# Kernel tuning notes

Measured on AMD Instinct MI355X. Metric: run time of the kernel, lower is better.

Reference implementation:

```python
import jax, jax.numpy as jnp
import numpy as np

D_MODEL = 1024
HEADS = 16
D_K = D_MODEL // HEADS
B, S = 4, 2048


def setup_inputs() -> dict:
    key = jax.random.key(0)
    ks = jax.random.split(key, 12)
    xav = float(np.sqrt(6.0 / (D_MODEL + D_MODEL)))  # xavier_uniform bound
    inp = {
        "query": jax.random.normal(ks[0], (B, S, D_MODEL), jnp.float32),
        "key": jax.random.normal(ks[1], (B, S, D_MODEL), jnp.float32),
        "value": jax.random.normal(ks[2], (B, S, D_MODEL), jnp.float32),
        # causal mask, broadcast over batch and heads: [1,1,S,S]
        "mask": jnp.tril(jnp.ones((S, S), jnp.int32))[None, None],
        "Wq": jax.random.uniform(ks[3], (D_MODEL, D_MODEL), jnp.float32, -xav, xav),
        "bq": jnp.zeros((D_MODEL,), jnp.float32),
        "Wk": jax.random.uniform(ks[4], (D_MODEL, D_MODEL), jnp.float32, -xav, xav),
        "bk": jnp.zeros((D_MODEL,), jnp.float32),
        "Wv": jax.random.uniform(ks[5], (D_MODEL, D_MODEL), jnp.float32, -xav, xav),
        "bv": jnp.zeros((D_MODEL,), jnp.float32),
        "Wo": jax.random.uniform(ks[6], (D_MODEL, D_MODEL), jnp.float32, -xav, xav),
        "bo": jnp.zeros((D_MODEL,), jnp.float32),
    }
    return inp


def reference(query, key, value, mask, Wq, bq, Wk, bk, Wv, bv, Wo, bo):
    b, s, d = query.shape
    # torch Linear: y = x @ W.T + b, W is [out, in]
    Q = (jnp.einsum("bsd,ed->bse", query, Wq) + bq).reshape(b, s, HEADS, D_K).transpose(0, 2, 1, 3)
    K = (jnp.einsum("bsd,ed->bse", key, Wk) + bk).reshape(b, -1, HEADS, D_K).transpose(0, 2, 1, 3)
    V = (jnp.einsum("bsd,ed->bse", value, Wv) + bv).reshape(b, -1, HEADS, D_K).transpose(0, 2, 1, 3)
    scale = 1.0 / jnp.sqrt(jnp.asarray(D_K, query.dtype))
    scores = jnp.einsum("bhqd,bhkd->bhqk", Q, K) * scale  # [B,H,S,S]
    scores = jnp.where(mask == 0, -jnp.inf, scores)
    attn = jax.nn.softmax(scores, axis=-1)
    attn = jnp.where(jnp.isnan(attn), jnp.zeros_like(attn), attn)  # nan-fix as in source
    out = jnp.einsum("bhqk,bhkd->bhqd", attn, V)
    out = out.transpose(0, 2, 1, 3).reshape(b, s, d)
    return jnp.einsum("bsd,ed->bse", out, Wo) + bo
```

## Files before the change

kernel.cpp:

```cpp
#include <hip/hip_runtime.h>
#include <hip/hip_bf16.h>

#define DM 1024
#define NHEADS 16
#define DKH 64
#define BATCH 4
#define SEQ 2048
#define MROWS (BATCH*SEQ)

typedef __attribute__((ext_vector_type(8))) short bf16x8;
typedef __attribute__((ext_vector_type(4))) short bf16x4;
typedef __attribute__((ext_vector_type(4))) float f32x4;

#if __has_builtin(__builtin_amdgcn_exp2f)
#define EXP2(x) __builtin_amdgcn_exp2f(x)
#else
#define EXP2(x) exp2f(x)
#endif

__device__ __forceinline__ unsigned short f2bf(float f){
  unsigned u = __float_as_uint(f);
  u += 0x7fffu + ((u >> 16) & 1u);
  return (unsigned short)(u >> 16);
}

__device__ __forceinline__ void gload16(const unsigned short* g, unsigned short* l){
  __builtin_amdgcn_global_load_lds((const __attribute__((address_space(1))) void*)g,
                                   (__attribute__((address_space(3))) void*)l, 16, 0, 0);
}

struct ConvArgs { const float* src[7]; unsigned short* dst[7]; };

__global__ __launch_bounds__(256) void conv_all(ConvArgs a){
  const int bx = blockIdx.x;
  int t, boff;
  if (bx < 24576){ t = bx >> 13; boff = bx & 8191; }
  else { int j = bx - 24576; t = 3 + (j >> 10); boff = j & 1023; }
  const float* __restrict__ src = a.src[t];
  unsigned short* __restrict__ dst = a.dst[t];
  const int i = (boff * 256 + threadIdx.x) * 4;
  const float4 v = *reinterpret_cast<const float4*>(src + i);
  ushort4 o;
  o.x = f2bf(v.x); o.y = f2bf(v.y); o.z = f2bf(v.z); o.w = f2bf(v.w);
  *reinterpret_cast<ushort4*>(dst + i) = o;
}

template<int MODE>
__global__ __launch_bounds__(256)
void gemm_bt(const unsigned short* __restrict__ A, const unsigned short* __restrict__ Bw,
             const float* __restrict__ bias, void* __restrict__ out, float scale)
{
  const int K = 1024;
  __shared__ short a_sh[128*64];
  __shared__ short b_sh[128*64];
  const int tid  = threadIdx.x;
  const int lane = tid & 63;
  const int wid  = tid >> 6;
  const int wm = wid >> 1, wn = wid & 1;
  const int tileM = blockIdx.x * 128;
  const int tileN = blockIdx.y * 128;

  f32x4 acc[4][4];
  #pragma unroll
  for (int i = 0; i < 4; i++)
    #pragma unroll
    for (int j = 0; j < 4; j++)
      acc[i][j] = (f32x4){0.f,0.f,0.f,0.f};

  const int lr = lane & 15;
  const int lg = lane >> 4;

  for (int k0 = 0; k0 < K; k0 += 64){
    bf16x8 ra[4], rb[4];
    #pragma unroll
    for (int i = 0; i < 4; i++){
      int v   = tid + 256*i;
      int row = v >> 3;
      int cg  = v & 7;
      ra[i] = *reinterpret_cast<const bf16x8*>(A  + (size_t)(tileM+row)*K + k0 + cg*8);
      rb[i] = *reinterpret_cast<const bf16x8*>(Bw + (size_t)(tileN+row)*K + k0 + cg*8);
    }
    __syncthreads();
    #pragma unroll
    for (int i = 0; i < 4; i++){
      int v   = tid + 256*i;
      int row = v >> 3;
      int cg  = v & 7;
      *reinterpret_cast<bf16x8*>(&a_sh[row*64 + ((cg ^ (row & 7)) * 8)]) = ra[i];
      *reinterpret_cast<bf16x8*>(&b_sh[row*64 + ((cg ^ (row & 7)) * 8)]) = rb[i];
    }
    __syncthreads();
    #pragma unroll
    for (int kk = 0; kk < 64; kk += 32){
      bf16x8 af[4], bfr[4];
      const int g0 = lg + (kk >> 3);
      #pragma unroll
      for (int fm = 0; fm < 4; fm++){
        int row = wm*64 + fm*16 + lr;
        af[fm] = *reinterpret_cast<const bf16x8*>(&a_sh[row*64 + ((g0 ^ (row & 7)) * 8)]);
      }
      #pragma unroll
      for (int fn = 0; fn < 4; fn++){
        int row = wn*64 + fn*16 + lr;
        bfr[fn] = *reinterpret_cast<const bf16x8*>(&b_sh[row*64 + ((g0 ^ (row & 7)) * 8)]);
      }
      #pragma unroll
      for (int fm = 0; fm < 4; fm++)
        #pragma unroll
        for (int fn = 0; fn < 4; fn++)
          acc[fm][fn] = __builtin_amdgcn_mfma_f32_16x16x32_bf16(af[fm], bfr[fn], acc[fm][fn], 0, 0, 0);
    }
  }

  #pragma unroll
  for (int fm = 0; fm < 4; fm++){
    #pragma unroll
    for (int fn = 0; fn < 4; fn++){
      #pragma unroll
      for (int r = 0; r < 4; r++){
        int m = tileM + wm*64 + fm*16 + lg*4 + r;
        int n = tileN + wn*64 + fn*16 + lr;
        float val = acc[fm][fn][r] + bias[n];
        if (MODE == 0){
          val *= scale;
          int b = m >> 11, s = m & 2047, h = n >> 6, d = n & 63;
          ((unsigned short*)out)[(((size_t)(b*NHEADS + h)*SEQ + s)*DKH + d)] = f2bf(val);
        } else if (MODE == 1){
          int b = m >> 11, s = m & 2047, h = n >> 6, d = n & 63;
          ((unsigned short*)out)[(((size_t)(b*NHEADS + h)*DKH + d)*SEQ + s)] = f2bf(val);
        } else {
          ((float*)out)[(size_t)m*DM + n] = val;
        }
      }
    }
  }
}

__global__ __launch_bounds__(256)
void attn_kernel(const unsigned short* __restrict__ Q, const unsigned short* __restrict__ Kb,
                 const unsigned short* __restrict__ Vt, unsigned short* __restrict__ Oout)
{
  __shared__ unsigned short k_sh[2][64*64];
  __shared__ unsigned short v_sh[2][64*64];
  const int lane = threadIdx.x & 63;
  const int w    = threadIdx.x >> 6;
  const int lr = lane & 15, grp = lane >> 4;
  const int bh = blockIdx.x;
  const int qtile = 15 - (int)blockIdx.y;
  const int qb0 = qtile * 128;
  const int qw0 = qb0 + w * 32;
  const int b = bh >> 4, h = bh & 15;
  const size_t kbase = (size_t)bh * SEQ * DKH;
  const size_t vbase = (size_t)bh * DKH * SEQ;

  const int r8 = lane >> 3, c8 = lane & 7;
  const int rowS0 = w*16 + r8;
  const int rowS1 = w*16 + 8 + r8;
  const size_t offK0 = (size_t)rowS0*DKH  + (size_t)((c8 ^ (rowS0 & 7)) * 8);
  const size_t offK1 = (size_t)rowS1*DKH  + (size_t)((c8 ^ (rowS1 & 7)) * 8);
  const size_t offV0 = (size_t)rowS0*SEQ  + (size_t)((c8 ^ (rowS0 & 7)) * 8);
  const size_t offV1 = (size_t)rowS1*SEQ  + (size_t)((c8 ^ (rowS1 & 7)) * 8);
  const int ldsA = (w*16)*64;
  const int ldsB = (w*16+8)*64;

  bf16x8 qf[2][2];
  #pragma unroll
  for (int qg = 0; qg < 2; qg++){
    size_t off = kbase + (size_t)(qw0 + qg*16 + lr)*DKH + grp*8;
    qf[qg][0] = *reinterpret_cast<const bf16x8*>(Q + off);
    qf[qg][1] = *reinterpret_cast<const bf16x8*>(Q + off + 32);
  }

  bf16x4 ones4;
  ones4[0] = (short)0x3F80; ones4[1] = (short)0x3F80;
  ones4[2] = (short)0x3F80; ones4[3] = (short)0x3F80;

  float mrun[2] = {-__builtin_inff(), -__builtin_inff()};
  f32x4 ls[2];
  f32x4 o[2][4];
  #pragma unroll
  for (int qg = 0; qg < 2; qg++){
    ls[qg] = (f32x4){0.f,0.f,0.f,0.f};
    #pragma unroll
    for (int dc = 0; dc < 4; dc++) o[qg][dc] = (f32x4){0.f,0.f,0.f,0.f};
  }

  const int nkb = qb0/64 + 2;

#define STAGE(kb_, bf_) do { \
    gload16(Kb + kbase + (size_t)(kb_)*4096 + offK0, (unsigned short*)&k_sh[bf_][ldsA]); \
    gload16(Kb + kbase + (size_t)(kb_)*4096 + offK1, (unsigned short*)&k_sh[bf_][ldsB]); \
    gload16(Vt + vbase + (size_t)(kb_)*64   + offV0, (unsigned short*)&v_sh[bf_][ldsA]); \
    gload16(Vt + vbase + (size_t)(kb_)*64   + offV1, (unsigned short*)&v_sh[bf_][ldsB]); \
  } while(0)

  STAGE(0, 0);
  __syncthreads();

  for (int kb = 0; kb < nkb; kb++){
    const int buf = kb & 1;
    if (kb + 1 < nkb) STAGE(kb + 1, buf ^ 1);

    if (kb*64 <= qw0 + 31){
      const unsigned short* ks = k_sh[buf];
      const unsigned short* vs = v_sh[buf];
      const bool act0 = (kb*64 <= qw0 + 15);

      f32x4 st[2][4];
      __builtin_amdgcn_s_setprio(1);
      #pragma unroll
      for (int ksub = 0; ksub < 4; ksub++){
        int rowk = ksub*16 + lr;
        bf16x8 kf0 = *reinterpret_cast<const bf16x8*>(&ks[rowk*64 + ((grp ^ (rowk & 7)) * 8)]);
        bf16x8 kf1 = *reinterpret_cast<const bf16x8*>(&ks[rowk*64 + (((4 + grp) ^ (rowk & 7)) * 8)]);
        #pragma unroll
        for (int qg = 0; qg < 2; qg++){
          f32x4 s = (f32x4){0.f,0.f,0.f,0.f};
          s = __builtin_amdgcn_mfma_f32_16x16x32_bf16(kf0, qf[qg][0], s, 0, 0, 0);
          s = __builtin_amdgcn_mfma_f32_16x16x32_bf16(kf1, qf[qg][1], s, 0, 0, 0);
          st[qg][ksub] = s;
        }
      }
      __builtin_amdgcn_s_setprio(0);

      bf16x4 pb[2][4];
      #pragma unroll
      for (int qg = 0; qg < 2; qg++){
        if (qg == 0 && !act0) continue;
        const int qgb = qw0 + qg*16;
        if (kb*64 + 63 > qgb){
          #pragma unroll
          for (int ksub = 0; ksub < 4; ksub++)
            #pragma unroll
            for (int r = 0; r < 4; r++){
              int kg = kb*64 + ksub*16 + grp*4 + r;
              if (kg > qgb + lr) st[qg][ksub][r] = -__builtin_inff();
            }
        }
        float mt = fmaxf(fmaxf(st[qg][0][0], st[qg][0][1]), fmaxf(st[qg][0][2], st[qg][0][3]));
        #pragma unroll
        for (int ksub = 1; ksub < 4; ksub++){
          mt = fmaxf(mt, fmaxf(fmaxf(st[qg][ksub][0], st[qg][ksub][1]),
                               fmaxf(st[qg][ksub][2], st[qg][ksub][3])));
        }
        mt = fmaxf(mt, __shfl_xor(mt, 16));
        mt = fmaxf(mt, __shfl_xor(mt, 32));
        const float mnew = fmaxf(mrun[qg], mt);
        const float corr = EXP2(mrun[qg] - mnew);
        mrun[qg] = mnew;
        #pragma unroll
        for (int dc = 0; dc < 4; dc++){
          o[qg][dc][0] *= corr; o[qg][dc][1] *= corr;
          o[qg][dc][2] *= corr; o[qg][dc][3] *= corr;
        }
        ls[qg][0] *= corr;
        #pragma unroll
        for (int ksub = 0; ksub < 4; ksub++){
          float p0 = EXP2(st[qg][ksub][0] - mnew);
          float p1 = EXP2(st[qg][ksub][1] - mnew);
          float p2 = EXP2(st[qg][ksub][2] - mnew);
          float p3 = EXP2(st[qg][ksub][3] - mnew);
          pb[qg][ksub][0] = (short)f2bf(p0);
          pb[qg][ksub][1] = (short)f2bf(p1);
          pb[qg][ksub][2] = (short)f2bf(p2);
          pb[qg][ksub][3] = (short)f2bf(p3);
        }
      }

      __builtin_amdgcn_s_setprio(1);
      #pragma unroll
      for (int ksub = 0; ksub < 4; ksub++){
        #pragma unroll
        for (int dc = 0; dc < 4; dc++){
          int rowd = dc*16 + lr;
          int cg16 = ksub*2 + (grp >> 1);
          bf16x4 vf = *reinterpret_cast<const bf16x4*>(
              &vs[rowd*64 + ((cg16 ^ (rowd & 7)) * 8) + (grp & 1)*4]);
          if (act0) o[0][dc] = __builtin_amdgcn_mfma_f32_16x16x16bf16_1k(vf, pb[0][ksub], o[0][dc], 0, 0, 0);
          o[1][dc] = __builtin_amdgcn_mfma_f32_16x16x16bf16_1k(vf, pb[1][ksub], o[1][dc], 0, 0, 0);
        }
        if (act0) ls[0] = __builtin_amdgcn_mfma_f32_16x16x16bf16_1k(ones4, pb[0][ksub], ls[0], 0, 0, 0);
        ls[1] = __builtin_amdgcn_mfma_f32_16x16x16bf16_1k(ones4, pb[1][ksub], ls[1], 0, 0, 0);
      }
      __builtin_amdgcn_s_setprio(0);
    }
    __syncthreads();
  }
#undef STAGE

  #pragma unroll
  for (int qg = 0; qg < 2; qg++){
    float inv = 1.0f / ls[qg][0];
    int qglob = qw0 + qg*16 + lr;
    size_t ob = ((size_t)(b*SEQ + qglob))*DM + h*DKH;
    #pragma unroll
    for (int dc = 0; dc < 4; dc++){
      ushort4 pk;
      pk.x = f2bf(o[qg][dc][0]*inv);
      pk.y = f2bf(o[qg][dc][1]*inv);
      pk.z = f2bf(o[qg][dc][2]*inv);
      pk.w = f2bf(o[qg][dc][3]*inv);
      *reinterpret_cast<ushort4*>(&Oout[ob + dc*16 + grp*4]) = pk;
    }
  }
}

extern "C" void kernel_launch(void* const* d_in, const int* in_sizes, int n_in,
                              void* d_out, int out_size, void* d_ws, size_t ws_size,
                              hipStream_t stream) {
  const float* query = (const float*)d_in[0];
  const float* key   = (const float*)d_in[1];
  const float* value = (const float*)d_in[2];
  const float* Wq = (const float*)d_in[4];
  const float* bq = (const float*)d_in[5];
  const float* Wk = (const float*)d_in[6];
  const float* bk = (const float*)d_in[7];
  const float* Wv = (const float*)d_in[8];
  const float* bv = (const float*)d_in[9];
  const float* Wo = (const float*)d_in[10];
  const float* bo = (const float*)d_in[11];
  float* out = (float*)d_out;

  char* ws = (char*)d_ws;
  const size_t SZ_X = (size_t)MROWS * DM * 2;
  const size_t SZ_W = (size_t)DM * DM * 2;
  unsigned short* qb  = (unsigned short*)(ws + 0);
  unsigned short* kb  = (unsigned short*)(ws + SZ_X);
  unsigned short* vb  = (unsigned short*)(ws + 2*SZ_X);
  unsigned short* wqb = (unsigned short*)(ws + 3*SZ_X);
  unsigned short* wkb = (unsigned short*)(ws + 3*SZ_X + SZ_W);
  unsigned short* wvb = (unsigned short*)(ws + 3*SZ_X + 2*SZ_W);
  unsigned short* wob = (unsigned short*)(ws + 3*SZ_X + 3*SZ_W);
  unsigned short* Vt  = (unsigned short*)(ws + 3*SZ_X + 4*SZ_W);
  unsigned short* Qb   = vb;
  unsigned short* Kbuf = qb;
  unsigned short* attO = kb;

  ConvArgs ca;
  ca.src[0] = query; ca.src[1] = key; ca.src[2] = value;
  ca.src[3] = Wq; ca.src[4] = Wk; ca.src[5] = Wv; ca.src[6] = Wo;
  ca.dst[0] = qb; ca.dst[1] = kb; ca.dst[2] = vb;
  ca.dst[3] = wqb; ca.dst[4] = wkb; ca.dst[5] = wvb; ca.dst[6] = wob;
  conv_all<<<28672, 256, 0, stream>>>(ca);

  dim3 gg(MROWS/128, DM/128);
  const float qscale = 0.125f * 1.4426950408889634f;
  gemm_bt<1><<<gg, 256, 0, stream>>>(vb, wvb, bv, (void*)Vt,   1.0f);
  gemm_bt<0><<<gg, 256, 0, stream>>>(qb, wqb, bq, (void*)Qb,   qscale);
  gemm_bt<0><<<gg, 256, 0, stream>>>(kb, wkb, bk, (void*)Kbuf, 1.0f);

  attn_kernel<<<dim3(64, 16), 256, 0, stream>>>(Qb, Kbuf, Vt, attO);

  gemm_bt<2><<<gg, 256, 0, stream>>>(attO, wob, bo, (void*)out, 1.0f);
}
```

Before: 216.6 us.

## Fuse fp32-to-bf16 activation conversion into projection GEMM loads; restructure attention softmax loop

Stops converting the query/key/value activations to bf16 in a separate pass. The QKV projection GEMMs now read the fp32 activations directly and convert them in registers with packed bf16 conversions, which removes a large write-then-read round trip through memory. Only the weights go through the standalone conversion kernel, and the workspace layout is rearranged to match. The attention kernel also gets a launch-bounds occupancy hint, computes the scores one query group at a time to cut register pressure, and uses packed bf16 conversion for the probabilities. In exchange the GEMMs fetch twice as many activation bytes per tile.

```diff
diff --git a/kernel.cpp b/kernel.cpp
--- a/kernel.cpp
+++ b/kernel.cpp
@@ -24,18 +24,31 @@
   return (unsigned short)(u >> 16);
 }
 
+__device__ __forceinline__ unsigned pk2bf(float lo, float hi){
+  union { __hip_bfloat162 h; unsigned u; } c;
+  c.h = __float22bfloat162_rn(make_float2(lo, hi));
+  return c.u;
+}
+
+__device__ __forceinline__ bf16x8 cvtA8(float4 a, float4 b){
+  union { unsigned u[4]; bf16x8 v; } r;
+  r.u[0] = pk2bf(a.x, a.y);
+  r.u[1] = pk2bf(a.z, a.w);
+  r.u[2] = pk2bf(b.x, b.y);
+  r.u[3] = pk2bf(b.z, b.w);
+  return r.v;
+}
+
 __device__ __forceinline__ void gload16(const unsigned short* g, unsigned short* l){
   __builtin_amdgcn_global_load_lds((const __attribute__((address_space(1))) void*)g,
                                    (__attribute__((address_space(3))) void*)l, 16, 0, 0);
 }
 
-struct ConvArgs { const float* src[7]; unsigned short* dst[7]; };
-
-__global__ __launch_bounds__(256) void conv_all(ConvArgs a){
-  const int bx = blockIdx.x;
-  int t, boff;
-  if (bx < 24576){ t = bx >> 13; boff = bx & 8191; }
-  else { int j = bx - 24576; t = 3 + (j >> 10); boff = j & 1023; }
+struct ConvArgs { const float* src[4]; unsigned short* dst[4]; };
+
+__global__ __launch_bounds__(256) void conv_w(ConvArgs a){
+  const int t = blockIdx.x >> 10;
+  const int boff = blockIdx.x & 1023;
   const float* __restrict__ src = a.src[t];
   unsigned short* __restrict__ dst = a.dst[t];
   const int i = (boff * 256 + threadIdx.x) * 4;
@@ -45,9 +58,9 @@
   *reinterpret_cast<ushort4*>(dst + i) = o;
 }
 
-template<int MODE>
+template<int MODE, int AFP32>
 __global__ __launch_bounds__(256)
-void gemm_bt(const unsigned short* __restrict__ A, const unsigned short* __restrict__ Bw,
+void gemm_bt(const void* __restrict__ Av, const unsigned short* __restrict__ Bw,
              const float* __restrict__ bias, void* __restrict__ out, float scale)
 {
   const int K = 1024;
@@ -77,7 +90,14 @@
       int v   = tid + 256*i;
       int row = v >> 3;
       int cg  = v & 7;
-      ra[i] = *reinterpret_cast<const bf16x8*>(A  + (size_t)(tileM+row)*K + k0 + cg*8);
+      if constexpr (AFP32){
+        const float* Af = (const float*)Av;
+        const float4 f0 = *reinterpret_cast<const float4*>(Af + (size_t)(tileM+row)*K + k0 + cg*8);
+        const float4 f1 = *reinterpret_cast<const float4*>(Af + (size_t)(tileM+row)*K + k0 + cg*8 + 4);
+        ra[i] = cvtA8(f0, f1);
+      } else {
+        ra[i] = *reinterpret_cast<const bf16x8*>((const unsigned short*)Av + (size_t)(tileM+row)*K + k0 + cg*8);
+      }
       rb[i] = *reinterpret_cast<const bf16x8*>(Bw + (size_t)(tileN+row)*K + k0 + cg*8);
     }
     __syncthreads();
@@ -136,7 +156,7 @@
   }
 }
 
-__global__ __launch_bounds__(256)
+__global__ __launch_bounds__(256, 4)
 void attn_kernel(const unsigned short* __restrict__ Q, const unsigned short* __restrict__ Kb,
                  const unsigned short* __restrict__ Vt, unsigned short* __restrict__ Oout)
 {
@@ -206,27 +226,24 @@
       const unsigned short* vs = v_sh[buf];
       const bool act0 = (kb*64 <= qw0 + 15);
 
-      f32x4 st[2][4];
-      __builtin_amdgcn_s_setprio(1);
-      #pragma unroll
-      for (int ksub = 0; ksub < 4; ksub++){
-        int rowk = ksub*16 + lr;
-        bf16x8 kf0 = *reinterpret_cast<const bf16x8*>(&ks[rowk*64 + ((grp ^ (rowk & 7)) * 8)]);
-        bf16x8 kf1 = *reinterpret_cast<const bf16x8*>(&ks[rowk*64 + (((4 + grp) ^ (rowk & 7)) * 8)]);
-        #pragma unroll
-        for (int qg = 0; qg < 2; qg++){
+      bf16x4 pb[2][4];
+      #pragma unroll
+      for (int qg = 0; qg < 2; qg++){
+        if (qg == 0 && !act0) continue;
+        f32x4 st[4];
+        __builtin_amdgcn_s_setprio(1);
+        #pragma unroll
+        for (int ksub = 0; ksub < 4; ksub++){
+          int rowk = ksub*16 + lr;
+          bf16x8 kf0 = *reinterpret_cast<const bf16x8*>(&ks[rowk*64 + ((grp ^ (rowk & 7)) * 8)]);
+          bf16x8 kf1 = *reinterpret_cast<const bf16x8*>(&ks[rowk*64 + (((4 + grp) ^ (rowk & 7)) * 8)]);
           f32x4 s = (f32x4){0.f,0.f,0.f,0.f};
           s = __builtin_amdgcn_mfma_f32_16x16x32_bf16(kf0, qf[qg][0], s, 0, 0, 0);
           s = __builtin_amdgcn_mfma_f32_16x16x32_bf16(kf1, qf[qg][1], s, 0, 0, 0);
-          st[qg][ksub] = s;
-        }
-      }
-      __builtin_amdgcn_s_setprio(0);
-
-      bf16x4 pb[2][4];
-      #pragma unroll
-      for (int qg = 0; qg < 2; qg++){
-        if (qg == 0 && !act0) continue;
+          st[ksub] = s;
+        }
+        __builtin_amdgcn_s_setprio(0);
+
         const int qgb = qw0 + qg*16;
         if (kb*64 + 63 > qgb){
           #pragma unroll
@@ -234,14 +251,14 @@
             #pragma unroll
             for (int r = 0; r < 4; r++){
               int kg = kb*64 + ksub*16 + grp*4 + r;
-              if (kg > qgb + lr) st[qg][ksub][r] = -__builtin_inff();
+              if (kg > qgb + lr) st[ksub][r] = -__builtin_inff();
             }
         }
-        float mt = fmaxf(fmaxf(st[qg][0][0], st[qg][0][1]), fmaxf(st[qg][0][2], st[qg][0][3]));
+        float mt = fmaxf(fmaxf(st[0][0], st[0][1]), fmaxf(st[0][2], st[0][3]));
         #pragma unroll
         for (int ksub = 1; ksub < 4; ksub++){
-          mt = fmaxf(mt, fmaxf(fmaxf(st[qg][ksub][0], st[qg][ksub][1]),
-                               fmaxf(st[qg][ksub][2], st[qg][ksub][3])));
+          mt = fmaxf(mt, fmaxf(fmaxf(st[ksub][0], st[ksub][1]),
+                               fmaxf(st[ksub][2], st[ksub][3])));
         }
         mt = fmaxf(mt, __shfl_xor(mt, 16));
         mt = fmaxf(mt, __shfl_xor(mt, 32));
@@ -256,14 +273,14 @@
         ls[qg][0] *= corr;
         #pragma unroll
         for (int ksub = 0; ksub < 4; ksub++){
-          float p0 = EXP2(st[qg][ksub][0] - mnew);
-          float p1 = EXP2(st[qg][ksub][1] - mnew);
-          float p2 = EXP2(st[qg][ksub][2] - mnew);
-          float p3 = EXP2(st[qg][ksub][3] - mnew);
-          pb[qg][ksub][0] = (short)f2bf(p0);
-          pb[qg][ksub][1] = (short)f2bf(p1);
-          pb[qg][ksub][2] = (short)f2bf(p2);
-          pb[qg][ksub][3] = (short)f2bf(p3);
+          float p0 = EXP2(st[ksub][0] - mnew);
+          float p1 = EXP2(st[ksub][1] - mnew);
+          float p2 = EXP2(st[ksub][2] - mnew);
+          float p3 = EXP2(st[ksub][3] - mnew);
+          union { unsigned u[2]; bf16x4 v; } pk;
+          pk.u[0] = pk2bf(p0, p1);
+          pk.u[1] = pk2bf(p2, p3);
+          pb[qg][ksub] = pk.v;
         }
       }
 
@@ -324,32 +341,27 @@
   char* ws = (char*)d_ws;
   const size_t SZ_X = (size_t)MROWS * DM * 2;
   const size_t SZ_W = (size_t)DM * DM * 2;
-  unsigned short* qb  = (unsigned short*)(ws + 0);
-  unsigned short* kb  = (unsigned short*)(ws + SZ_X);
-  unsigned short* vb  = (unsigned short*)(ws + 2*SZ_X);
-  unsigned short* wqb = (unsigned short*)(ws + 3*SZ_X);
-  unsigned short* wkb = (unsigned short*)(ws + 3*SZ_X + SZ_W);
-  unsigned short* wvb = (unsigned short*)(ws + 3*SZ_X + 2*SZ_W);
-  unsigned short* wob = (unsigned short*)(ws + 3*SZ_X + 3*SZ_W);
-  unsigned short* Vt  = (unsigned short*)(ws + 3*SZ_X + 4*SZ_W);
-  unsigned short* Qb   = vb;
-  unsigned short* Kbuf = qb;
-  unsigned short* attO = kb;
+  unsigned short* wqb = (unsigned short*)(ws + 0);
+  unsigned short* wkb = (unsigned short*)(ws + SZ_W);
+  unsigned short* wvb = (unsigned short*)(ws + 2*SZ_W);
+  unsigned short* wob = (unsigned short*)(ws + 3*SZ_W);
+  unsigned short* Qb   = (unsigned short*)(ws + 4*SZ_W);
+  unsigned short* Kbuf = (unsigned short*)(ws + 4*SZ_W + SZ_X);
+  unsigned short* Vt   = (unsigned short*)(ws + 4*SZ_W + 2*SZ_X);
+  unsigned short* attO = (unsigned short*)(ws + 4*SZ_W + 3*SZ_X);
 
   ConvArgs ca;
-  ca.src[0] = query; ca.src[1] = key; ca.src[2] = value;
-  ca.src[3] = Wq; ca.src[4] = Wk; ca.src[5] = Wv; ca.src[6] = Wo;
-  ca.dst[0] = qb; ca.dst[1] = kb; ca.dst[2] = vb;
-  ca.dst[3] = wqb; ca.dst[4] = wkb; ca.dst[5] = wvb; ca.dst[6] = wob;
-  conv_all<<<28672, 256, 0, stream>>>(ca);
+  ca.src[0] = Wq; ca.src[1] = Wk; ca.src[2] = Wv; ca.src[3] = Wo;
+  ca.dst[0] = wqb; ca.dst[1] = wkb; ca.dst[2] = wvb; ca.dst[3] = wob;
+  conv_w<<<4096, 256, 0, stream>>>(ca);
 
   dim3 gg(MROWS/128, DM/128);
   const float qscale = 0.125f * 1.4426950408889634f;
-  gemm_bt<1><<<gg, 256, 0, stream>>>(vb, wvb, bv, (void*)Vt,   1.0f);
-  gemm_bt<0><<<gg, 256, 0, stream>>>(qb, wqb, bq, (void*)Qb,   qscale);
-  gemm_bt<0><<<gg, 256, 0, stream>>>(kb, wkb, bk, (void*)Kbuf, 1.0f);
+  gemm_bt<1,1><<<gg, 256, 0, stream>>>(value, wvb, bv, (void*)Vt,   1.0f);
+  gemm_bt<0,1><<<gg, 256, 0, stream>>>(query, wqb, bq, (void*)Qb,   qscale);
+  gemm_bt<0,1><<<gg, 256, 0, stream>>>(key,   wkb, bk, (void*)Kbuf, 1.0f);
 
   attn_kernel<<<dim3(64, 16), 256, 0, stream>>>(Qb, Kbuf, Vt, attO);
 
-  gemm_bt<2><<<gg, 256, 0, stream>>>(attO, wob, bo, (void*)out, 1.0f);
-}
+  gemm_bt<2,0><<<gg, 256, 0, stream>>>(attO, wob, bo, (void*)out, 1.0f);
+}
```

New measurement: 200.1 us. 7.6% less time.
